# Performance work log

Hardware: AMD Instinct MI355X
Metric: run time of the kernel (lower is better)

## Reference

```python
import jax, jax.numpy as jnp
import numpy as np

B, M, D = 512, 128, 512
N_ITER = 400      # FISTA iterations for batched NNLS (converges well past scipy nnls tol here)
POW_ITERS = 30    # power-iteration steps for spectral norm (Lipschitz constant)


def setup_inputs() -> dict:
    key = jax.random.key(0)
    k1, k2 = jax.random.split(key)
    pred_cost = jax.random.normal(k1, (B, D), dtype=jnp.float32)
    tight_ctrs = jax.random.normal(k2, (B, M, D), dtype=jnp.float32)
    return {"pred_cost": pred_cost, "tight_ctrs": tight_ctrs}


def _spectral_norm(G):
    # G: (B, M, M) PSD Gram matrices; power iteration -> largest eigenvalue per sample
    v = jnp.ones(G.shape[:-1], G.dtype)  # (B, M)
    def body(v, _):
        v = jnp.einsum('bij,bj->bi', G, v)
        v = v / (jnp.linalg.norm(v, axis=-1, keepdims=True) + 1e-12)
        return v, None
    v, _ = jax.lax.scan(body, v, None, length=POW_ITERS)
    Gv = jnp.einsum('bij,bj->bi', G, v)
    return jnp.linalg.norm(Gv, axis=-1)  # (B,)


def _batched_nnls(G, b, step):
    # Solve per-sample: min_{lam>=0} 0.5 lam^T G lam - b^T lam  (== ||ctr^T lam - p||^2 up to const)
    # FISTA with nonnegativity projection. G: (B,M,M), b: (B,M), step: (B,)
    lam0 = jnp.zeros_like(b)
    def body(carry, _):
        lam, y, t = carry
        grad = jnp.einsum('bij,bj->bi', G, y) - b
        lam_new = jnp.maximum(y - step[:, None] * grad, 0.0)
        t_new = 0.5 * (1.0 + jnp.sqrt(1.0 + 4.0 * t * t))
        y_new = lam_new + ((t - 1.0) / t_new) * (lam_new - lam)
        return (lam_new, y_new, t_new), None
    (lam, _, _), _ = jax.lax.scan(body, (lam0, lam0, jnp.float32(1.0)), None, length=N_ITER)
    return lam


def reference(pred_cost, tight_ctrs):
    # optmodel.modelSense == MINIMIZE -> flip sign of predicted cost
    p = -pred_cost  # (B, D)
    # drop (mask to zero) near-zero constraint rows: ctr[np.abs(ctr).sum(axis=1) > 1e-7]
    row_mask = jnp.sum(jnp.abs(tight_ctrs), axis=-1) > 1e-7  # (B, M)
    ctr = tight_ctrs * row_mask[..., None].astype(tight_ctrs.dtype)
    # NNLS: min_{lam>=0} ||ctr.T @ lam - p||^2, batched via normal equations
    G = jnp.einsum('bmd,bnd->bmn', ctr, ctr)   # (B, M, M)
    b = jnp.einsum('bmd,bd->bm', ctr, p)       # (B, M)
    L = _spectral_norm(G)
    step = 1.0 / jnp.maximum(L, 1e-12)
    lam = _batched_nnls(G, b, step)            # (B, M), lam >= 0
    proj = jnp.einsum('bm,bmd->bd', lam, ctr)  # (B, D) projection onto the cone
    proj = proj / (jnp.linalg.norm(proj, axis=-1, keepdims=True) + 1e-12)
    # projection is computed on detached numpy in the original -> constant wrt autograd
    proj = jax.lax.stop_gradient(proj)
    # loss = -cosine_similarity(p, proj), torch eps = 1e-8
    eps = jnp.float32(1e-8)
    pn = jnp.maximum(jnp.linalg.norm(p, axis=-1), eps)
    qn = jnp.maximum(jnp.linalg.norm(proj, axis=-1), eps)
    cos = jnp.sum(p * proj, axis=-1) / (pn * qn)
    return jnp.mean(-cos)  # reduction='mean'
```

## Files before the change

### kernel.cpp

```cpp
#include <hip/hip_runtime.h>
#include <math.h>

#define BATCH 512
#define M 128
#define D 512
#define PITER 12
#define NRUN 72
#define KC 32
#define NCH (D / KC)
#define SSTR 36
#define SCL 0.0009765625f

typedef __attribute__((ext_vector_type(8))) _Float16 h8;
typedef __attribute__((ext_vector_type(4))) _Float16 h4;
typedef __attribute__((ext_vector_type(4))) float f4;
typedef __attribute__((ext_vector_type(2))) float v2f;

union H8u { h8 v; h4 q[2]; };

__device__ __forceinline__ float rdlane(float v, int k) {
    return __builtin_bit_cast(float, __builtin_amdgcn_readlane(__builtin_bit_cast(int, v), k));
}

__launch_bounds__(1024, 4)
__global__ void build_kernel(const float* __restrict__ pred,
                             const float* __restrict__ ctr,
                             float* __restrict__ Gw,
                             float* __restrict__ bw,
                             float* __restrict__ pw)
{
    __shared__ __align__(16) _Float16 hiS[2][M * SSTR];
    __shared__ __align__(16) _Float16 loS[2][M * SSTR];
    __shared__ __align__(16) float p_s[D];
    __shared__ float mask_s[M];
    __shared__ float wred[16];

    const int tid = threadIdx.x;
    const int blk = blockIdx.x;
    const int w = tid >> 6, l = tid & 63;
    const int row = tid >> 3;
    const int seg = tid & 7;
    const int kk = 4 * seg;
    const int a = w >> 2;
    const int bcol = w & 3;
    const int fm = l & 15;
    const int fq = l >> 4;

    const float* predRow = pred + (size_t)blk * D;
    const float* ctrBase = ctr + (size_t)blk * (size_t)(M * D);

    float pv = (tid < D) ? predRow[tid] : 0.0f;
    if (tid < D) p_s[tid] = pv;
    float v = pv * pv;
    #pragma unroll
    for (int off = 32; off > 0; off >>= 1) v += __shfl_xor(v, off, 64);
    if (l == 0) wred[w] = v;
    __syncthreads();
    if (tid == 0) {
        float s = 0.0f;
        #pragma unroll
        for (int i = 0; i < 16; ++i) s += wred[i];
        pw[blk] = s;
    }

    f4 acc[2][2];
    #pragma unroll
    for (int i = 0; i < 2; ++i)
        #pragma unroll
        for (int jx = 0; jx < 2; ++jx)
            acc[i][jx] = (f4)0.0f;

    float rs = 0.0f, bp = 0.0f;
    const float* src = ctrBase + (size_t)row * D + kk;
    float4 f = *(const float4*)(src);

    for (int kc = 0; kc < NCH; ++kc) {
        const int cc = kc & 1;
        _Float16 hx = (_Float16)f.x, hy = (_Float16)f.y,
                 hz = (_Float16)f.z, hw = (_Float16)f.w;
        h4 hv = {hx, hy, hz, hw};
        h4 lv = {(_Float16)(f.x - (float)hx), (_Float16)(f.y - (float)hy),
                 (_Float16)(f.z - (float)hz), (_Float16)(f.w - (float)hw)};
        *(h4*)(hiS[cc] + row * SSTR + kk) = hv;
        *(h4*)(loS[cc] + row * SSTR + kk) = lv;
        rs += fabsf(f.x) + fabsf(f.y) + fabsf(f.z) + fabsf(f.w);
        {
            float4 pp = *(const float4*)(p_s + kc * KC + kk);
            bp += f.x * pp.x + f.y * pp.y + f.z * pp.z + f.w * pp.w;
        }
        __syncthreads();
        if (kc + 1 < NCH) f = *(const float4*)(src + (kc + 1) * KC);

        h8 Ah[2], Al[2], Bh[2], Bl[2];
        #pragma unroll
        for (int t = 0; t < 2; ++t) {
            {
                const _Float16* p = hiS[cc] + (16 * (2 * a + t) + fm) * SSTR + 8 * fq;
                H8u u; u.q[0] = *(const h4*)(p); u.q[1] = *(const h4*)(p + 4);
                Ah[t] = u.v;
            }
            {
                const _Float16* p = loS[cc] + (16 * (2 * a + t) + fm) * SSTR + 8 * fq;
                H8u u; u.q[0] = *(const h4*)(p); u.q[1] = *(const h4*)(p + 4);
                Al[t] = u.v;
            }
            {
                const _Float16* p = hiS[cc] + (16 * (2 * bcol + t) + fm) * SSTR + 8 * fq;
                H8u u; u.q[0] = *(const h4*)(p); u.q[1] = *(const h4*)(p + 4);
                Bh[t] = u.v;
            }
            {
                const _Float16* p = loS[cc] + (16 * (2 * bcol + t) + fm) * SSTR + 8 * fq;
                H8u u; u.q[0] = *(const h4*)(p); u.q[1] = *(const h4*)(p + 4);
                Bl[t] = u.v;
            }
        }
        #pragma unroll
        for (int al = 0; al < 2; ++al)
            #pragma unroll
            for (int be = 0; be < 2; ++be) {
                acc[al][be] = __builtin_amdgcn_mfma_f32_16x16x32_f16(Ah[al], Bh[be], acc[al][be], 0, 0, 0);
                acc[al][be] = __builtin_amdgcn_mfma_f32_16x16x32_f16(Ah[al], Bl[be], acc[al][be], 0, 0, 0);
                acc[al][be] = __builtin_amdgcn_mfma_f32_16x16x32_f16(Al[al], Bh[be], acc[al][be], 0, 0, 0);
            }
    }

    rs += __shfl_xor(rs, 1, 64);
    rs += __shfl_xor(rs, 2, 64);
    rs += __shfl_xor(rs, 4, 64);
    bp += __shfl_xor(bp, 1, 64);
    bp += __shfl_xor(bp, 2, 64);
    bp += __shfl_xor(bp, 4, 64);
    if (seg == 0) {
        bool ok = rs > 1e-7f;
        mask_s[row] = ok ? 1.0f : 0.0f;
        bw[(size_t)blk * M + row] = ok ? -bp : 0.0f;
    }
    __syncthreads();

    float* Gb = Gw + (size_t)blk * (M * M);
    float mc0 = mask_s[32 * bcol + fm];
    float mc1 = mask_s[32 * bcol + 16 + fm];
    #pragma unroll
    for (int al = 0; al < 2; ++al)
        #pragma unroll
        for (int r = 0; r < 4; ++r) {
            const int grow = 32 * a + 16 * al + 4 * fq + r;
            const float mr_ = mask_s[grow];
            Gb[(size_t)grow * M + 32 * bcol + fm]      = acc[al][0][r] * mr_ * mc0;
            Gb[(size_t)grow * M + 32 * bcol + 16 + fm] = acc[al][1][r] * mr_ * mc1;
        }
}

__launch_bounds__(64, 1)
__global__ void solve_kernel(const float* __restrict__ Gw,
                             const float* __restrict__ bw,
                             const float* __restrict__ pw,
                             float* __restrict__ out)
{
    const int l = threadIdx.x;
    const int blk = blockIdx.x;

    const float* g0 = Gw + (size_t)blk * (M * M) + (size_t)l * M;
    const float* g1 = g0 + (size_t)64 * M;
    v2f g2a[64], g2b[64];
    #pragma unroll
    for (int u = 0; u < 16; ++u) {
        f4 x = *(const f4*)(g0 + 4 * u);
        f4 y = *(const f4*)(g1 + 4 * u);
        g2a[4 * u + 0] = v2f{x.x, y.x}; g2a[4 * u + 1] = v2f{x.y, y.y};
        g2a[4 * u + 2] = v2f{x.z, y.z}; g2a[4 * u + 3] = v2f{x.w, y.w};
    }
    #pragma unroll
    for (int u = 0; u < 16; ++u) {
        f4 x = *(const f4*)(g0 + 64 + 4 * u);
        f4 y = *(const f4*)(g1 + 64 + 4 * u);
        g2b[4 * u + 0] = v2f{x.x, y.x}; g2b[4 * u + 1] = v2f{x.y, y.y};
        g2b[4 * u + 2] = v2f{x.z, y.z}; g2b[4 * u + 3] = v2f{x.w, y.w};
    }
    const float b0 = bw[(size_t)blk * M + l];
    const float b1 = bw[(size_t)blk * M + 64 + l];

    auto matvec = [&](float ylo, float yhi) -> v2f {
        v2f acc[8];
        #pragma unroll
        for (int i = 0; i < 8; ++i) acc[i] = v2f{0.0f, 0.0f};
        #pragma unroll
        for (int k = 0; k < 64; ++k) {
            float s0 = rdlane(ylo, k);
            float s1 = rdlane(yhi, k);
            acc[k & 3]       += g2a[k] * v2f{s0, s0};
            acc[4 + (k & 3)] += g2b[k] * v2f{s1, s1};
        }
        return ((acc[0] + acc[1]) + (acc[2] + acc[3]))
             + ((acc[4] + acc[5]) + (acc[6] + acc[7]));
    };

    auto waveSum = [&](float x) -> float {
        #pragma unroll
        for (int off = 32; off > 0; off >>= 1) x += __shfl_xor(x, off, 64);
        return x;
    };

    float vlo = 1.0f, vhi = 1.0f;
    for (int it = 0; it < PITER; ++it) {
        v2f u = matvec(vlo, vhi);
        vlo = u.x * SCL; vhi = u.y * SCL;
    }
    float step;
    {
        v2f u = matvec(vlo, vhi);
        float nv = waveSum(vlo * vlo + vhi * vhi);
        float nu = waveSum(u.x * u.x + u.y * u.y);
        float L = sqrtf(nu / fmaxf(nv, 1e-30f));
        step = 1.0f / fmaxf(1.12f * L, 1e-12f);
    }

    v2f st2 = v2f{step, step};
    #pragma unroll
    for (int k = 0; k < 64; ++k) { g2a[k] *= st2; g2b[k] *= st2; }
    const float bs0 = step * b0, bs1 = step * b1;

    float lam0 = 0.0f, lam1 = 0.0f, y0 = 0.0f, y1 = 0.0f, tk = 1.0f;
    for (int it = 0; it < NRUN; ++it) {
        v2f u = matvec(y0, y1);
        float tkn = 0.5f * (1.0f + sqrtf(1.0f + 4.0f * tk * tk));
        float bet = (tk - 1.0f) / tkn;
        float n0 = fmaxf(y0 - u.x + bs0, 0.0f);
        float n1 = fmaxf(y1 - u.y + bs1, 0.0f);
        y0 = n0 + bet * (n0 - lam0);
        y1 = n1 + bet * (n1 - lam1);
        lam0 = n0; lam1 = n1; tk = tkn;
    }

    {
        v2f u = matvec(lam0, lam1);
        float sg = waveSum(lam0 * u.x + lam1 * u.y);
        float sb = waveSum(lam0 * b0 + lam1 * b1);
        if (l == 0) {
            float glg = sg / step;
            float np_ = sqrtf(fmaxf(glg, 0.0f));
            float pdot = sb / (np_ + 1e-12f);
            float qn = fmaxf(np_ / (np_ + 1e-12f), 1e-8f);
            float pn = fmaxf(sqrtf(pw[blk]), 1e-8f);
            float c = pdot / (pn * qn);
            atomicAdd(out, -c * (1.0f / (float)BATCH));
        }
    }
}

extern "C" void kernel_launch(void* const* d_in, const int* in_sizes, int n_in,
                              void* d_out, int out_size, void* d_ws, size_t ws_size,
                              hipStream_t stream) {
    const float* pred = (const float*)d_in[0];
    const float* ctr  = (const float*)d_in[1];
    float* out = (float*)d_out;

    float* Gw = (float*)d_ws;
    float* bw = Gw + (size_t)BATCH * M * M;
    float* pw = bw + (size_t)BATCH * M;

    hipMemsetAsync(out, 0, sizeof(float), stream);
    build_kernel<<<BATCH, 1024, 0, stream>>>(pred, ctr, Gw, bw, pw);
    solve_kernel<<<BATCH, 64, 0, stream>>>(Gw, bw, pw, out);
}
```

Baseline: 268.8 us.

## Drop fp16 split-precision correction terms, double K chunk, fold memset into build kernel

The Gram matrix build now uses a single fp16 MFMA per tile instead of the hi/lo three-product compensation, removing the low-part shared buffer and two thirds of the MFMAs. The K chunk is doubled to 64 with 8-element vector loads and h8 LDS reads, which halves the number of barriers. The output zeroing memset is replaced by a write inside the build kernel. The cost is a loss of precision in G, which may affect the solver's accuracy.

```diff
diff --git a/kernel.cpp b/kernel.cpp
--- a/kernel.cpp
+++ b/kernel.cpp
@@ -6,17 +6,14 @@
 #define D 512
 #define PITER 12
 #define NRUN 72
-#define KC 32
+#define KC 64
 #define NCH (D / KC)
-#define SSTR 36
+#define SSTR 72
 #define SCL 0.0009765625f
 
 typedef __attribute__((ext_vector_type(8))) _Float16 h8;
-typedef __attribute__((ext_vector_type(4))) _Float16 h4;
 typedef __attribute__((ext_vector_type(4))) float f4;
 typedef __attribute__((ext_vector_type(2))) float v2f;
-
-union H8u { h8 v; h4 q[2]; };
 
 __device__ __forceinline__ float rdlane(float v, int k) {
     return __builtin_bit_cast(float, __builtin_amdgcn_readlane(__builtin_bit_cast(int, v), k));
@@ -27,10 +24,10 @@
                              const float* __restrict__ ctr,
                              float* __restrict__ Gw,
                              float* __restrict__ bw,
-                             float* __restrict__ pw)
+                             float* __restrict__ pw,
+                             float* __restrict__ out)
 {
     __shared__ __align__(16) _Float16 hiS[2][M * SSTR];
-    __shared__ __align__(16) _Float16 loS[2][M * SSTR];
     __shared__ __align__(16) float p_s[D];
     __shared__ float mask_s[M];
     __shared__ float wred[16];
@@ -40,11 +37,13 @@
     const int w = tid >> 6, l = tid & 63;
     const int row = tid >> 3;
     const int seg = tid & 7;
-    const int kk = 4 * seg;
+    const int kk = 8 * seg;
     const int a = w >> 2;
     const int bcol = w & 3;
     const int fm = l & 15;
     const int fq = l >> 4;
+
+    if (blk == 0 && tid == 0) out[0] = 0.0f;
 
     const float* predRow = pred + (size_t)blk * D;
     const float* ctrBase = ctr + (size_t)blk * (size_t)(M * D);
@@ -72,57 +71,42 @@
 
     float rs = 0.0f, bp = 0.0f;
     const float* src = ctrBase + (size_t)row * D + kk;
-    float4 f = *(const float4*)(src);
+    float4 f0 = *(const float4*)(src);
+    float4 f1 = *(const float4*)(src + 4);
 
     for (int kc = 0; kc < NCH; ++kc) {
         const int cc = kc & 1;
-        _Float16 hx = (_Float16)f.x, hy = (_Float16)f.y,
-                 hz = (_Float16)f.z, hw = (_Float16)f.w;
-        h4 hv = {hx, hy, hz, hw};
-        h4 lv = {(_Float16)(f.x - (float)hx), (_Float16)(f.y - (float)hy),
-                 (_Float16)(f.z - (float)hz), (_Float16)(f.w - (float)hw)};
-        *(h4*)(hiS[cc] + row * SSTR + kk) = hv;
-        *(h4*)(loS[cc] + row * SSTR + kk) = lv;
-        rs += fabsf(f.x) + fabsf(f.y) + fabsf(f.z) + fabsf(f.w);
+        h8 hv = {(_Float16)f0.x, (_Float16)f0.y, (_Float16)f0.z, (_Float16)f0.w,
+                 (_Float16)f1.x, (_Float16)f1.y, (_Float16)f1.z, (_Float16)f1.w};
+        *(h8*)(hiS[cc] + row * SSTR + kk) = hv;
+        rs += (fabsf(f0.x) + fabsf(f0.y) + fabsf(f0.z) + fabsf(f0.w))
+            + (fabsf(f1.x) + fabsf(f1.y) + fabsf(f1.z) + fabsf(f1.w));
         {
-            float4 pp = *(const float4*)(p_s + kc * KC + kk);
-            bp += f.x * pp.x + f.y * pp.y + f.z * pp.z + f.w * pp.w;
+            float4 pp0 = *(const float4*)(p_s + kc * KC + kk);
+            float4 pp1 = *(const float4*)(p_s + kc * KC + kk + 4);
+            bp += f0.x * pp0.x + f0.y * pp0.y + f0.z * pp0.z + f0.w * pp0.w
+                + f1.x * pp1.x + f1.y * pp1.y + f1.z * pp1.z + f1.w * pp1.w;
         }
         __syncthreads();
-        if (kc + 1 < NCH) f = *(const float4*)(src + (kc + 1) * KC);
-
-        h8 Ah[2], Al[2], Bh[2], Bl[2];
-        #pragma unroll
-        for (int t = 0; t < 2; ++t) {
-            {
-                const _Float16* p = hiS[cc] + (16 * (2 * a + t) + fm) * SSTR + 8 * fq;
-                H8u u; u.q[0] = *(const h4*)(p); u.q[1] = *(const h4*)(p + 4);
-                Ah[t] = u.v;
+        if (kc + 1 < NCH) {
+            f0 = *(const float4*)(src + (kc + 1) * KC);
+            f1 = *(const float4*)(src + (kc + 1) * KC + 4);
+        }
+
+        #pragma unroll
+        for (int ks = 0; ks < 2; ++ks) {
+            h8 Ah[2], Bh[2];
+            #pragma unroll
+            for (int t = 0; t < 2; ++t) {
+                Ah[t] = *(const h8*)(hiS[cc] + (16 * (2 * a + t) + fm) * SSTR + 32 * ks + 8 * fq);
+                Bh[t] = *(const h8*)(hiS[cc] + (16 * (2 * bcol + t) + fm) * SSTR + 32 * ks + 8 * fq);
             }
-            {
-                const _Float16* p = loS[cc] + (16 * (2 * a + t) + fm) * SSTR + 8 * fq;
-                H8u u; u.q[0] = *(const h4*)(p); u.q[1] = *(const h4*)(p + 4);
-                Al[t] = u.v;
-            }
-            {
-                const _Float16* p = hiS[cc] + (16 * (2 * bcol + t) + fm) * SSTR + 8 * fq;
-                H8u u; u.q[0] = *(const h4*)(p); u.q[1] = *(const h4*)(p + 4);
-                Bh[t] = u.v;
-            }
-            {
-                const _Float16* p = loS[cc] + (16 * (2 * bcol + t) + fm) * SSTR + 8 * fq;
-                H8u u; u.q[0] = *(const h4*)(p); u.q[1] = *(const h4*)(p + 4);
-                Bl[t] = u.v;
-            }
-        }
-        #pragma unroll
-        for (int al = 0; al < 2; ++al)
             #pragma unroll
-            for (int be = 0; be < 2; ++be) {
-                acc[al][be] = __builtin_amdgcn_mfma_f32_16x16x32_f16(Ah[al], Bh[be], acc[al][be], 0, 0, 0);
-                acc[al][be] = __builtin_amdgcn_mfma_f32_16x16x32_f16(Ah[al], Bl[be], acc[al][be], 0, 0, 0);
-                acc[al][be] = __builtin_amdgcn_mfma_f32_16x16x32_f16(Al[al], Bh[be], acc[al][be], 0, 0, 0);
-            }
+            for (int al = 0; al < 2; ++al)
+                #pragma unroll
+                for (int be = 0; be < 2; ++be)
+                    acc[al][be] = __builtin_amdgcn_mfma_f32_16x16x32_f16(Ah[al], Bh[be], acc[al][be], 0, 0, 0);
+        }
     }
 
     rs += __shfl_xor(rs, 1, 64);
@@ -260,7 +244,6 @@
     float* bw = Gw + (size_t)BATCH * M * M;
     float* pw = bw + (size_t)BATCH * M;
 
-    hipMemsetAsync(out, 0, sizeof(float), stream);
-    build_kernel<<<BATCH, 1024, 0, stream>>>(pred, ctr, Gw, bw, pw);
+    build_kernel<<<BATCH, 1024, 0, stream>>>(pred, ctr, Gw, bw, pw, out);
     solve_kernel<<<BATCH, 64, 0, stream>>>(Gw, bw, pw, out);
 }
```

After: 263.9 us. No clear change (-1.8%).
